# Performance work log

Hardware: AMD Instinct MI355X
Metric: run time of the kernel (lower is better)

Reference implementation:

```python
import jax, jax.numpy as jnp
import numpy as np

D_MODEL = 2048
NUM_HEADS = 16
HEAD_DIM = D_MODEL // NUM_HEADS
LAYER_IDX = 0
NUM_LAYERS = 13
REINIT_LAMBDA = 0.8


def setup_inputs() -> dict:
    key = jax.random.key(0)
    ks = jax.random.split(key, 8)
    B, S = 2, 2048
    x = jax.random.normal(ks[0], (B, S, D_MODEL), dtype=jnp.float32)
    init = 1.0 / np.sqrt(D_MODEL)
    def w(k):
        return jax.random.uniform(k, (D_MODEL, D_MODEL), dtype=jnp.float32, minval=-init, maxval=init)
    lam_init = REINIT_LAMBDA * ((LAYER_IDX + 1) / NUM_LAYERS)
    return {
        "x": x,
        "q1_w": w(ks[1]), "k1_w": w(ks[2]),
        "q2_w": w(ks[3]), "k2_w": w(ks[4]),
        "v_w": w(ks[5]), "o_w": w(ks[6]),
        "lambda_param": jnp.full((NUM_HEADS,), lam_init, dtype=jnp.float32),
    }


def _heads(t, B, S):
    # [B, S, D] -> [B, H, S, Dh]
    return t.reshape(B, S, NUM_HEADS, HEAD_DIM).transpose(0, 2, 1, 3)


def reference(x, q1_w, k1_w, q2_w, k2_w, v_w, o_w, lambda_param):
    B, S, _ = x.shape
    # nn.Linear(bias=False): y = x @ W.T, W is [out, in]
    q1 = _heads(x @ q1_w.T, B, S)
    k1 = _heads(x @ k1_w.T, B, S)
    q2 = _heads(x @ q2_w.T, B, S)
    k2 = _heads(x @ k2_w.T, B, S)
    v = _heads(x @ v_w.T, B, S)
    scale = jnp.sqrt(jnp.float32(HEAD_DIM))
    attn1 = jax.nn.softmax(jnp.einsum('bhqd,bhkd->bhqk', q1, k1) / scale, axis=-1)
    attn2 = jax.nn.softmax(jnp.einsum('bhqd,bhkd->bhqk', q2, k2) / scale, axis=-1)
    lam = lambda_param.reshape(1, NUM_HEADS, 1, 1)
    out = jnp.einsum('bhqk,bhkd->bhqd', attn1 - lam * attn2, v)
    out = out.transpose(0, 2, 1, 3).reshape(B, S, D_MODEL)
    return out @ o_w.T
```

## Files before the change

kernel.cpp:

```cpp
#include <hip/hip_runtime.h>
#include <hip/hip_bf16.h>
#include <stdint.h>

typedef __bf16 bf16_t;
typedef __bf16 bf16x8 __attribute__((ext_vector_type(8)));
typedef float f32x4 __attribute__((ext_vector_type(4)));

#define D_MODEL 2048
#define SEQ     2048
#define NHEADS  16
#define HDIM    128
#define BATCH   2
#define NTOK    (BATCH * SEQ)
#define NELEM   ((size_t)BATCH * SEQ * D_MODEL)
#define D2      ((size_t)D_MODEL * D_MODEL)

__global__ void __launch_bounds__(256)
cvt7_kernel(const float* __restrict__ x,
            const float* __restrict__ w0, const float* __restrict__ w1,
            const float* __restrict__ w2, const float* __restrict__ w3,
            const float* __restrict__ w4, const float* __restrict__ w5,
            bf16_t* __restrict__ xb, bf16_t* __restrict__ wb) {
  const int y = blockIdx.y;
  const float* srcs[7] = {x, w0, w1, w2, w3, w4, w5};
  const float* src = srcs[y];
  bf16_t* dst = (y == 0) ? xb : wb + (size_t)(y - 1) * D2;
  const size_t n = (y == 0) ? NELEM : D2;
  const size_t base = ((size_t)blockIdx.x * 256 + threadIdx.x) * 8;
  if (base >= n) return;
  f32x4 lo = *(const f32x4*)(src + base);
  f32x4 hi = *(const f32x4*)(src + base + 4);
  union { bf16x8 v; bf16_t h[8]; } u;
#pragma unroll
  for (int j = 0; j < 4; j++) {
    u.h[j]     = (bf16_t)lo[j];
    u.h[j + 4] = (bf16_t)hi[j];
  }
  *(bf16x8*)(dst + base) = u.v;
}

__device__ __forceinline__ void async_load16(const void* g, void* l) {
  __builtin_amdgcn_global_load_lds(
      (const __attribute__((address_space(1))) void*)g,
      (__attribute__((address_space(3))) void*)l, 16, 0, 0);
}

template <int TRANS, typename TC>
__device__ __forceinline__ void gemm_tile_body(const bf16_t* __restrict__ A,
                                               const bf16_t* __restrict__ W,
                                               TC* __restrict__ C) {
  extern __shared__ bf16_t smem[];
  bf16_t* As = smem;
  bf16_t* Bs = smem + 128 * 32;
  const int K = D_MODEL, N = D_MODEL;
  const int tid  = threadIdx.x;
  const int wave = tid >> 6, lane = tid & 63;
  const int quad = lane >> 4, l16 = lane & 15;
  const int tm = blockIdx.x * 128, tn = blockIdx.y * 128;
  const int wm = (wave & 1) * 64, wn = (wave >> 1) * 64;

  f32x4 acc[4][4];
#pragma unroll
  for (int i = 0; i < 4; i++)
#pragma unroll
    for (int j = 0; j < 4; j++) acc[i][j] = (f32x4){0.f, 0.f, 0.f, 0.f};

  const int srow = lane >> 2;
  const int scol = (lane & 3) * 8;

  for (int k0 = 0; k0 < K; k0 += 32) {
    __syncthreads();
#pragma unroll
    for (int i = 0; i < 2; i++) {
      const int rbase = (i * 4 + wave) * 16;
      async_load16(A + (size_t)(tm + rbase + srow) * K + k0 + scol, As + rbase * 32);
      async_load16(W + (size_t)(tn + rbase + srow) * K + k0 + scol, Bs + rbase * 32);
    }
    __syncthreads();

    bf16x8 af[4], bfr[4];
#pragma unroll
    for (int i = 0; i < 4; i++)
      af[i] = *(const bf16x8*)(As + (wm + i * 16 + l16) * 32 + quad * 8);
#pragma unroll
    for (int j = 0; j < 4; j++)
      bfr[j] = *(const bf16x8*)(Bs + (wn + j * 16 + l16) * 32 + quad * 8);
#pragma unroll
    for (int i = 0; i < 4; i++)
#pragma unroll
      for (int j = 0; j < 4; j++)
        acc[i][j] = __builtin_amdgcn_mfma_f32_16x16x32_bf16(af[i], bfr[j], acc[i][j], 0, 0, 0);
  }

#pragma unroll
  for (int i = 0; i < 4; i++) {
    const int r0 = wm + i * 16 + quad * 4;
#pragma unroll
    for (int j = 0; j < 4; j++) {
      const int c = tn + wn + j * 16 + l16;
      if constexpr (TRANS) {
        const int m = tm + r0;
        const int b = m >> 11;
        const int s = m & (SEQ - 1);
        union { bf16_t h[4]; uint2 u2; } p;
#pragma unroll
        for (int r = 0; r < 4; r++) p.h[r] = (bf16_t)acc[i][j][r];
        *(uint2*)((bf16_t*)C + (size_t)(b * D_MODEL + c) * SEQ + s) = p.u2;
      } else {
#pragma unroll
        for (int r = 0; r < 4; r++)
          C[(size_t)(tm + r0 + r) * N + c] = (TC)acc[i][j][r];
      }
    }
  }
}

__global__ void __launch_bounds__(256)
proj5_kernel(const bf16_t* __restrict__ xb, const bf16_t* __restrict__ wb,
             bf16_t* __restrict__ q1, bf16_t* __restrict__ k1,
             bf16_t* __restrict__ q2, bf16_t* __restrict__ k2,
             bf16_t* __restrict__ vt) {
  const bf16_t* w = wb + (size_t)blockIdx.z * D2;
  switch (blockIdx.z) {
    case 0: gemm_tile_body<0, bf16_t>(xb, w, q1); break;
    case 1: gemm_tile_body<0, bf16_t>(xb, w, k1); break;
    case 2: gemm_tile_body<0, bf16_t>(xb, w, q2); break;
    case 3: gemm_tile_body<0, bf16_t>(xb, w, k2); break;
    default: gemm_tile_body<1, bf16_t>(xb, w, vt); break;
  }
}

__global__ void __launch_bounds__(256)
gemm_out_kernel(const bf16_t* __restrict__ A, const bf16_t* __restrict__ W,
                float* __restrict__ C) {
  gemm_tile_body<0, float>(A, W, C);
}

__global__ void __launch_bounds__(256, 3)
diff_attn_kernel(const bf16_t* __restrict__ q1g, const bf16_t* __restrict__ k1g,
                 const bf16_t* __restrict__ q2g, const bf16_t* __restrict__ k2g,
                 const bf16_t* __restrict__ vtg, const float* __restrict__ lamg,
                 bf16_t* __restrict__ outg) {
  const int blk = blockIdx.x;
  const int xcd = blk & 7;
  const int idx = blk >> 3;
  const int bh  = xcd * 4 + (idx >> 5);
  const int qt  = idx & 31;
  const int b = bh >> 4, h = bh & 15;
  const int tid = threadIdx.x, wave = tid >> 6, lane = tid & 63;
  const int quad = lane >> 4, l16 = lane & 15;
  const int q0 = qt * 64 + wave * 16;

  __shared__ bf16_t K1s[64 * 128];
  __shared__ bf16_t K2s[64 * 128];
  __shared__ bf16_t Vs[128 * 64];

  const bf16_t* q1p = q1g + ((size_t)b * SEQ + q0) * D_MODEL + h * HDIM;
  const bf16_t* q2p = q2g + ((size_t)b * SEQ + q0) * D_MODEL + h * HDIM;
  const bf16_t* k1p = k1g + (size_t)b * SEQ * D_MODEL + h * HDIM;
  const bf16_t* k2p = k2g + (size_t)b * SEQ * D_MODEL + h * HDIM;
  const bf16_t* vtp = vtg + ((size_t)b * D_MODEL + h * HDIM) * SEQ;

  bf16x8 aq1[4], aq2[4];
#pragma unroll
  for (int c = 0; c < 4; c++) {
    aq1[c] = *(const bf16x8*)(q1p + (size_t)l16 * D_MODEL + c * 32 + quad * 8);
    aq2[c] = *(const bf16x8*)(q2p + (size_t)l16 * D_MODEL + c * 32 + quad * 8);
  }

  f32x4 O1[8], O2[8];
#pragma unroll
  for (int n = 0; n < 8; n++) {
    O1[n] = (f32x4){0.f, 0.f, 0.f, 0.f};
    O2[n] = (f32x4){0.f, 0.f, 0.f, 0.f};
  }
  float l1 = 0.f, l2 = 0.f;

  const float c2 = 0.0883883476483184f * 1.4426950408889634f;

  const int k_r  = lane >> 4;
  const int k_p  = lane & 15;
  const int v_r  = lane >> 3;
  const int v_p  = lane & 7;

  for (int kt = 0; kt < SEQ; kt += 64) {
    __syncthreads();
#pragma unroll
    for (int i = 0; i < 4; i++) {
      const int krb = wave * 16 + i * 4;
      const int kr  = krb + k_r;
      const int kkey = (((kr >> 2) & 3) << 3) | (((kr >> 4) & 1) << 2) |
                       (kr & 3) | (kr & 32);
      const int kg = k_p ^ (kr & 7);
      async_load16(k1p + (size_t)(kt + kkey) * D_MODEL + kg * 8, K1s + krb * 128);
      async_load16(k2p + (size_t)(kt + kkey) * D_MODEL + kg * 8, K2s + krb * 128);
      const int vrb = wave * 32 + i * 8;
      const int vr  = vrb + v_r;
      const int vg  = v_p ^ (vr & 7);
      async_load16(vtp + (size_t)vr * SEQ + kt + vg * 8, Vs + vrb * 64);
    }
    __syncthreads();

    f32x4 s1[4], s2[4];
#pragma unroll
    for (int s = 0; s < 4; s++) {
      s1[s] = (f32x4){0.f, 0.f, 0.f, 0.f};
      s2[s] = (f32x4){0.f, 0.f, 0.f, 0.f};
    }
    const int xsw = l16 & 7;
#pragma unroll
    for (int c = 0; c < 4; c++) {
      const int pos = ((c * 4 + quad) ^ xsw) * 8;
#pragma unroll
      for (int s = 0; s < 4; s++) {
        const int rowoff = (s * 16 + l16) * 128;
        bf16x8 f1 = *(const bf16x8*)(K1s + rowoff + pos);
        bf16x8 f2 = *(const bf16x8*)(K2s + rowoff + pos);
        s1[s] = __builtin_amdgcn_mfma_f32_16x16x32_bf16(f1, aq1[c], s1[s], 0, 0, 0);
        s2[s] = __builtin_amdgcn_mfma_f32_16x16x32_bf16(f2, aq2[c], s2[s], 0, 0, 0);
      }
    }

#pragma unroll
    for (int half = 0; half < 2; half++) {
      union { bf16x8 v; bf16_t h[8]; } p1, p2;
#pragma unroll
      for (int r = 0; r < 4; r++) {
        const float e1a = __builtin_amdgcn_exp2f(s1[2 * half][r] * c2);
        const float e1b = __builtin_amdgcn_exp2f(s1[2 * half + 1][r] * c2);
        const float e2a = __builtin_amdgcn_exp2f(s2[2 * half][r] * c2);
        const float e2b = __builtin_amdgcn_exp2f(s2[2 * half + 1][r] * c2);
        p1.h[r] = (bf16_t)e1a; p1.h[4 + r] = (bf16_t)e1b;
        p2.h[r] = (bf16_t)e2a; p2.h[4 + r] = (bf16_t)e2b;
        l1 += e1a + e1b;
        l2 += e2a + e2b;
      }
      const int vpos = ((half * 4 + quad) ^ xsw) * 8;
#pragma unroll
      for (int n = 0; n < 8; n++) {
        bf16x8 vf = *(const bf16x8*)(Vs + (n * 16 + l16) * 64 + vpos);
        O1[n] = __builtin_amdgcn_mfma_f32_16x16x32_bf16(p1.v, vf, O1[n], 0, 0, 0);
        O2[n] = __builtin_amdgcn_mfma_f32_16x16x32_bf16(p2.v, vf, O2[n], 0, 0, 0);
      }
    }
  }

  l1 += __shfl_xor(l1, 16); l1 += __shfl_xor(l1, 32);
  l2 += __shfl_xor(l2, 16); l2 += __shfl_xor(l2, 32);

  const float lam = lamg[h];
  const float i1 = 1.f / l1, i2 = lam / l2;
  float i1o[4], i2o[4];
#pragma unroll
  for (int r = 0; r < 4; r++) {
    i1o[r] = __shfl(i1, quad * 4 + r, 16);
    i2o[r] = __shfl(i2, quad * 4 + r, 16);
  }
  bf16_t* op = outg + ((size_t)b * SEQ + q0) * D_MODEL + h * HDIM;
#pragma unroll
  for (int r = 0; r < 4; r++)
#pragma unroll
    for (int n = 0; n < 8; n++)
      op[(size_t)(quad * 4 + r) * D_MODEL + n * 16 + l16] =
          (bf16_t)(O1[n][r] * i1o[r] - O2[n][r] * i2o[r]);
}

extern "C" void kernel_launch(void* const* d_in, const int* in_sizes, int n_in,
                              void* d_out, int out_size, void* d_ws, size_t ws_size,
                              hipStream_t stream) {
  const float* x   = (const float*)d_in[0];
  const float* wq1 = (const float*)d_in[1];
  const float* wk1 = (const float*)d_in[2];
  const float* wq2 = (const float*)d_in[3];
  const float* wk2 = (const float*)d_in[4];
  const float* wv  = (const float*)d_in[5];
  const float* wo  = (const float*)d_in[6];
  const float* lam = (const float*)d_in[7];

  bf16_t* ws = (bf16_t*)d_ws;
  bf16_t* q1 = ws + 0 * NELEM;
  bf16_t* k1 = ws + 1 * NELEM;
  bf16_t* q2 = ws + 2 * NELEM;
  bf16_t* k2 = ws + 3 * NELEM;
  bf16_t* vt = ws + 4 * NELEM;
  bf16_t* xb = ws + 5 * NELEM;
  bf16_t* ao = xb;
  bf16_t* wb = ws + 6 * NELEM;

  cvt7_kernel<<<dim3(4096, 7), dim3(256), 0, stream>>>(
      x, wq1, wk1, wq2, wk2, wv, wo, xb, wb);
  proj5_kernel<<<dim3(NTOK / 128, D_MODEL / 128, 5), dim3(256), 16384, stream>>>(
      xb, wb, q1, k1, q2, k2, vt);
  diff_attn_kernel<<<dim3(BATCH * NHEADS * (SEQ / 64)), dim3(256), 0, stream>>>(
      q1, k1, q2, k2, vt, lam, ao);
  gemm_out_kernel<<<dim3(NTOK / 128, D_MODEL / 128), dim3(256), 16384, stream>>>(
      ao, wb + 5 * D2, (float*)d_out);
}
```

Measured before the change: 597.0 us.

## Rewrite projection GEMM as 256x256 tile with 8 waves and pipelined async LDS

Replaces the 128x128, 4-wave projection GEMM with a 256x256-tile, 8-wave kernel. It double-buffers 64-wide K slices in 128KB of LDS through async global-to-LDS loads, uses an XOR-swizzled LDS layout, and interleaves barriers, waitcnts and setprio around 16x16x32 MFMA groups. It also remaps block indices so each XCD gets contiguous tiles. The aim is higher MFMA utilisation and more operand reuse per byte loaded, at the cost of large LDS use, low occupancy and complex hand-scheduled synchronisation.

```diff
diff --git a/kernel.cpp b/kernel.cpp
--- a/kernel.cpp
+++ b/kernel.cpp
@@ -49,9 +49,9 @@
 __device__ __forceinline__ void gemm_tile_body(const bf16_t* __restrict__ A,
                                                const bf16_t* __restrict__ W,
                                                TC* __restrict__ C) {
-  extern __shared__ bf16_t smem[];
-  bf16_t* As = smem;
-  bf16_t* Bs = smem + 128 * 32;
+  extern __shared__ char smem[];
+  bf16_t* As = (bf16_t*)smem;
+  bf16_t* Bs = (bf16_t*)smem + 128 * 32;
   const int K = D_MODEL, N = D_MODEL;
   const int tid  = threadIdx.x;
   const int wave = tid >> 6, lane = tid & 63;
@@ -116,24 +116,177 @@
 }
 
 __global__ void __launch_bounds__(256)
+gemm_out_kernel(const bf16_t* __restrict__ A, const bf16_t* __restrict__ W,
+                float* __restrict__ C) {
+  gemm_tile_body<0, float>(A, W, C);
+}
+
+template <int TRANS, typename TC>
+__device__ __forceinline__ void gemm256_body(const bf16_t* __restrict__ A,
+                                             const bf16_t* __restrict__ W,
+                                             TC* __restrict__ C,
+                                             const int tm, const int tn) {
+  extern __shared__ char smem[];
+  constexpr int K = D_MODEL;
+  constexpr int NT = K / 64;
+  const int tid = threadIdx.x;
+  const int wid = tid >> 6, lane = tid & 63;
+  const int quad = lane >> 4, l16 = lane & 15;
+  const int wm = wid >> 2, wn = wid & 3;
+
+  const int sr = lane >> 2;
+  const int sc = (lane & 3) ^ ((lane >> 4) & 2);
+  const int rdoff = (l16 * 64 + quad * 16) ^ ((l16 & 8) << 2);
+
+  f32x4 acc[8][4];
+#pragma unroll
+  for (int i = 0; i < 8; i++)
+#pragma unroll
+    for (int j = 0; j < 4; j++) acc[i][j] = (f32x4){0.f, 0.f, 0.f, 0.f};
+
+  bf16x8 af[2][4], bfA[2][2], bfB[2][2];
+
+#define STAGE256(P, rowbase, ldsbase, h, t)                                      \
+  {                                                                              \
+    const bf16_t* _s = (P) + (size_t)((rowbase) + (h) * 128 + wid * 16 + sr) * K \
+                           + ((t) * 64 + sc * 8);                                \
+    char* _d = smem + (ldsbase) + (h) * 16384 + wid * 2048;                      \
+    async_load16(_s, _d);                                                        \
+    async_load16(_s + 32, _d + 1024);                                            \
+  }
+
+#define LDA256(c, rh)                                                            \
+  _Pragma("unroll") for (int ks = 0; ks < 2; ks++)                               \
+  _Pragma("unroll") for (int j = 0; j < 4; j++)                                  \
+      af[ks][j] = *(const bf16x8*)(smem + (c) * 65536 +                          \
+                  ((wm * 8 + (rh) * 4 + j) * 2 + ks) * 1024 + rdoff);
+
+#define LDB256(c, dst, cf0)                                                      \
+  _Pragma("unroll") for (int ks = 0; ks < 2; ks++)                               \
+  _Pragma("unroll") for (int j = 0; j < 2; j++)                                  \
+      dst[ks][j] = *(const bf16x8*)(smem + (c) * 65536 + 32768 +                 \
+                   ((wn * 4 + (cf0) + j) * 2 + ks) * 1024 + rdoff);
+
+#define MFMA16(rh, bfr, cb)                                                      \
+  _Pragma("unroll") for (int j = 0; j < 4; j++)                                  \
+  _Pragma("unroll") for (int cf = 0; cf < 2; cf++)                               \
+  _Pragma("unroll") for (int ks = 0; ks < 2; ks++)                               \
+      acc[(rh) * 4 + j][(cb) + cf] = __builtin_amdgcn_mfma_f32_16x16x32_bf16(    \
+          af[ks][j], bfr[ks][cf], acc[(rh) * 4 + j][(cb) + cf], 0, 0, 0);
+
+#define BAR256() __builtin_amdgcn_s_barrier()
+#define LGKM0()                                                                  \
+  { asm volatile("s_waitcnt lgkmcnt(0)" ::: "memory");                           \
+    __builtin_amdgcn_sched_barrier(0); }
+#define VMW4()                                                                   \
+  { asm volatile("s_waitcnt vmcnt(4)" ::: "memory");                             \
+    __builtin_amdgcn_sched_barrier(0); }
+#define VMW0()                                                                   \
+  { asm volatile("s_waitcnt vmcnt(0)" ::: "memory");                             \
+    __builtin_amdgcn_sched_barrier(0); }
+
+  STAGE256(A, tm, 0,     0, 0); STAGE256(A, tm, 0,     1, 0);
+  STAGE256(W, tn, 32768, 0, 0); STAGE256(W, tn, 32768, 1, 0);
+  STAGE256(W, tn, 98304, 0, 1); STAGE256(W, tn, 98304, 1, 1);
+  VMW4();
+  BAR256();
+
+  for (int it = 0; it < NT / 2; ++it) {
+    const int kt = 2 * it;
+    const int t2 = (kt + 2 < NT) ? kt + 2 : 0;
+    const int t3 = (kt + 3 < NT) ? kt + 3 : 0;
+
+    LDA256(0, 0); LDB256(0, bfA, 0);
+    STAGE256(A, tm, 65536, 0, kt + 1);
+    BAR256(); LGKM0();
+    __builtin_amdgcn_s_setprio(1); MFMA16(0, bfA, 0); __builtin_amdgcn_s_setprio(0);
+    BAR256();
+    LDB256(0, bfB, 2);
+    STAGE256(A, tm, 65536, 1, kt + 1);
+    BAR256(); LGKM0();
+    __builtin_amdgcn_s_setprio(1); MFMA16(0, bfB, 2); __builtin_amdgcn_s_setprio(0);
+    BAR256();
+    LDA256(0, 1);
+    STAGE256(W, tn, 32768, 0, t2);
+    BAR256(); LGKM0();
+    __builtin_amdgcn_s_setprio(1); MFMA16(1, bfA, 0); __builtin_amdgcn_s_setprio(0);
+    BAR256();
+    STAGE256(W, tn, 32768, 1, t2);
+    BAR256();
+    __builtin_amdgcn_s_setprio(1); MFMA16(1, bfB, 2); __builtin_amdgcn_s_setprio(0);
+    VMW4();
+    BAR256();
+    LDA256(1, 0); LDB256(1, bfA, 0);
+    STAGE256(A, tm, 0, 0, t2);
+    BAR256(); LGKM0();
+    __builtin_amdgcn_s_setprio(1); MFMA16(0, bfA, 0); __builtin_amdgcn_s_setprio(0);
+    BAR256();
+    LDB256(1, bfB, 2);
+    STAGE256(A, tm, 0, 1, t2);
+    BAR256(); LGKM0();
+    __builtin_amdgcn_s_setprio(1); MFMA16(0, bfB, 2); __builtin_amdgcn_s_setprio(0);
+    BAR256();
+    LDA256(1, 1);
+    STAGE256(W, tn, 98304, 0, t3);
+    BAR256(); LGKM0();
+    __builtin_amdgcn_s_setprio(1); MFMA16(1, bfA, 0); __builtin_amdgcn_s_setprio(0);
+    BAR256();
+    STAGE256(W, tn, 98304, 1, t3);
+    BAR256();
+    __builtin_amdgcn_s_setprio(1); MFMA16(1, bfB, 2); __builtin_amdgcn_s_setprio(0);
+    VMW4();
+    BAR256();
+  }
+  VMW0();
+
+#pragma unroll
+  for (int rf = 0; rf < 8; rf++) {
+    const int r0 = wm * 128 + rf * 16 + quad * 4;
+#pragma unroll
+    for (int cf = 0; cf < 4; cf++) {
+      const int c = tn + wn * 64 + cf * 16 + l16;
+      if constexpr (TRANS) {
+        const int m = tm + r0;
+        const int b = m >> 11;
+        const int s = m & (SEQ - 1);
+        union { bf16_t h[4]; uint2 u2; } p;
+#pragma unroll
+        for (int r = 0; r < 4; r++) p.h[r] = (bf16_t)acc[rf][cf][r];
+        *(uint2*)((bf16_t*)C + (size_t)(b * D_MODEL + c) * SEQ + s) = p.u2;
+      } else {
+#pragma unroll
+        for (int r = 0; r < 4; r++)
+          C[(size_t)(tm + r0 + r) * D_MODEL + c] = (TC)acc[rf][cf][r];
+      }
+    }
+  }
+#undef STAGE256
+#undef LDA256
+#undef LDB256
+#undef MFMA16
+#undef BAR256
+#undef LGKM0
+#undef VMW4
+#undef VMW0
+}
+
+__global__ void __launch_bounds__(512, 2)
 proj5_kernel(const bf16_t* __restrict__ xb, const bf16_t* __restrict__ wb,
              bf16_t* __restrict__ q1, bf16_t* __restrict__ k1,
              bf16_t* __restrict__ q2, bf16_t* __restrict__ k2,
              bf16_t* __restrict__ vt) {
-  const bf16_t* w = wb + (size_t)blockIdx.z * D2;
-  switch (blockIdx.z) {
-    case 0: gemm_tile_body<0, bf16_t>(xb, w, q1); break;
-    case 1: gemm_tile_body<0, bf16_t>(xb, w, k1); break;
-    case 2: gemm_tile_body<0, bf16_t>(xb, w, q2); break;
-    case 3: gemm_tile_body<0, bf16_t>(xb, w, k2); break;
-    default: gemm_tile_body<1, bf16_t>(xb, w, vt); break;
-  }
-}
-
-__global__ void __launch_bounds__(256)
-gemm_out_kernel(const bf16_t* __restrict__ A, const bf16_t* __restrict__ W,
-                float* __restrict__ C) {
-  gemm_tile_body<0, float>(A, W, C);
+  const int g = blockIdx.y;
+  const int orig = blockIdx.x;
+  const int wg = (orig & 7) * 16 + (orig >> 3);
+  const int tm = (wg & 15) * 256;
+  const int tn = (wg >> 4) * 256;
+  const bf16_t* w = wb + (size_t)g * D2;
+  if (g == 4) {
+    gemm256_body<1, bf16_t>(xb, w, vt, tm, tn);
+  } else {
+    bf16_t* o = (g == 0) ? q1 : (g == 1) ? k1 : (g == 2) ? q2 : k2;
+    gemm256_body<0, bf16_t>(xb, w, o, tm, tn);
+  }
 }
 
 __global__ void __launch_bounds__(256, 3)
@@ -287,9 +440,16 @@
   bf16_t* ao = xb;
   bf16_t* wb = ws + 6 * NELEM;
 
+  static bool attr_set = false;
+  if (!attr_set) {
+    (void)hipFuncSetAttribute(reinterpret_cast<const void*>(proj5_kernel),
+                              hipFuncAttributeMaxDynamicSharedMemorySize, 131072);
+    attr_set = true;
+  }
+
   cvt7_kernel<<<dim3(4096, 7), dim3(256), 0, stream>>>(
       x, wq1, wk1, wq2, wk2, wv, wo, xb, wb);
-  proj5_kernel<<<dim3(NTOK / 128, D_MODEL / 128, 5), dim3(256), 16384, stream>>>(
+  proj5_kernel<<<dim3(128, 5), dim3(512), 131072, stream>>>(
       xb, wb, q1, k1, q2, k2, vt);
   diff_attn_kernel<<<dim3(BATCH * NHEADS * (SEQ / 64)), dim3(256), 0, stream>>>(
       q1, k1, q2, k2, vt, lam, ao);
```

Result: faster. 570.7 us (-4.4%).
